# Kernel tuning notes

Measured on AMD Instinct MI355X. Metric: run time of the kernel, lower is better.

Reference implementation:

```python
import jax, jax.numpy as jnp
import numpy as np

VOCAB = 50000          # max binary columnId
N_NUM = 5000           # numerical feature ids = 1..5000
N_CAT = VOCAB + 1 - N_NUM  # categorical table rows (incl. padding row 0)
D = 128
B, L = 512, 512


def setup_inputs() -> dict:
    key = jax.random.key(0)
    k1, k2, k3, k4, k5 = jax.random.split(key, 5)
    feature_ids = jax.random.randint(k1, (B, L), 0, VOCAB + 1)
    feature_values = jax.random.normal(k2, (B, L), dtype=jnp.float32)
    cat_table = jax.random.normal(k3, (N_CAT, D), dtype=jnp.float32) * 0.02
    cat_table = cat_table.at[0].set(0.0)  # padding_idx=0
    num_weight = jax.random.normal(k4, (N_NUM, D), dtype=jnp.float32) * 0.02
    num_bias = jax.random.normal(k5, (N_NUM, D), dtype=jnp.float32) * 0.02
    # lookup buffers, exactly as built in __init__ with numerical ids = 1..N_NUM
    input_to_numeric = np.zeros(VOCAB + 1, dtype=np.int64)
    num_ids = np.arange(1, N_NUM + 1)
    input_to_numeric[num_ids] = np.arange(1, N_NUM + 1)
    input_to_categorical = np.zeros(VOCAB + 1, dtype=np.int64)
    cat_ids = np.where(input_to_numeric == 0)[0]
    input_to_categorical[cat_ids[1:]] = np.arange(1, cat_ids.size)
    return {
        "feature_ids": feature_ids,
        "feature_values": feature_values,
        "cat_table": cat_table,
        "num_weight": num_weight,
        "num_bias": num_bias,
        "input_to_numeric": jnp.asarray(input_to_numeric),
        "input_to_categorical": jnp.asarray(input_to_categorical),
    }


def reference(feature_ids, feature_values, cat_table, num_weight, num_bias,
              input_to_numeric, input_to_categorical):
    # numerical mask: isin(feature_ids, numerical_feature_ids) == nonzero mapped idx
    n_idx = input_to_numeric[feature_ids]                 # [B,L], 1..N_NUM or 0
    numerical_mask = n_idx > 0                            # [B,L]
    # numerical path: weight[id] * value + bias[id]  (1-based mapped -> 0-based row)
    n_row = jnp.maximum(n_idx - 1, 0)                     # [B,L]
    num_emb = num_weight[n_row] * feature_values[..., None] + num_bias[n_row]  # [B,L,D]
    # categorical path: route numerical positions to padding id 0
    cat_features = jnp.where(numerical_mask, 0, feature_ids)
    c_idx = input_to_categorical[cat_features]            # [B,L]
    cat_emb = cat_table[c_idx]                            # [B,L,D]
    # merge
    return jnp.where(numerical_mask[..., None], num_emb, cat_emb)
```

## Files before the change

kernel.cpp:

```cpp
#include <hip/hip_runtime.h>


constexpr int D  = 128;
constexpr int BL = 512 * 512;
constexpr int POS_PER_WAVE  = 16;
constexpr int WAVES_PER_BLK = 4;
constexpr int POS_PER_BLK   = POS_PER_WAVE * WAVES_PER_BLK;

__global__ __launch_bounds__(256) void emb_kernel(
    const int*    __restrict__ feature_ids,
    const float*  __restrict__ feature_values,
    const float*  __restrict__ cat_table,
    const float*  __restrict__ num_weight,
    const float*  __restrict__ num_bias,
    float*        __restrict__ out)
{
    const int tid  = threadIdx.x;
    const int lane = tid & 63;
    const int wave = tid >> 6;
    const int wbase = blockIdx.x * POS_PER_BLK + wave * POS_PER_WAVE;

    const int  myp = lane & 15;
    const int  id  = feature_ids[wbase + myp];
    const float mv = feature_values[wbase + myp];
    const int route = (id >= 1 && id <= 5000) ? -id
                    : ((id > 5000) ? id - 5000 : 0);

    const int sub  = (lane & 31) * 4;
    const int half = lane >> 5;

    float4 av[8];
    float  sc[8];
    int    brow[8];
#pragma unroll
    for (int k = 0; k < 8; ++k) {
        const int   p  = k * 2 + half;
        const int   rt = __shfl(route, p);
        const float vv = __shfl(mv, p);
        const bool isnum = rt < 0;
        const int  row   = isnum ? (-rt - 1) : rt;
        const float* a   = (isnum ? num_weight : cat_table) + row * D + sub;
        av[k]   = *(const float4*)a;
        sc[k]   = isnum ? vv : 1.0f;
        brow[k] = isnum ? row : -1;
    }

    float4 bv[8];
#pragma unroll
    for (int k = 0; k < 8; ++k) {
        bv[k] = make_float4(0.f, 0.f, 0.f, 0.f);
        if (brow[k] >= 0)
            bv[k] = *(const float4*)(num_bias + brow[k] * D + sub);
    }

    float* const obase = out + (long long)wbase * D;
#pragma unroll
    for (int k = 0; k < 8; ++k) {
        float4 r;
        r.x = fmaf(av[k].x, sc[k], bv[k].x);
        r.y = fmaf(av[k].y, sc[k], bv[k].y);
        r.z = fmaf(av[k].z, sc[k], bv[k].z);
        r.w = fmaf(av[k].w, sc[k], bv[k].w);
        *(float4*)(obase + (k * 64 + lane) * 4) = r;
    }
}

extern "C" void kernel_launch(void* const* d_in, const int* in_sizes, int n_in,
                              void* d_out, int out_size, void* d_ws, size_t ws_size,
                              hipStream_t stream) {
    const int*   feature_ids    = (const int*)  d_in[0];
    const float* feature_values = (const float*)d_in[1];
    const float* cat_table      = (const float*)d_in[2];
    const float* num_weight     = (const float*)d_in[3];
    const float* num_bias       = (const float*)d_in[4];
    float*       out            = (float*)      d_out;

    const int blocks = BL / POS_PER_BLK;
    emb_kernel<<<blocks, 256, 0, stream>>>(
        feature_ids, feature_values, cat_table, num_weight, num_bias, out);
}
```

Before: 178.8 us.

## Prefetch embedding tables into cache with grid barrier before persistent gather

Switches to a fixed grid of 1024 blocks, each handling 256 positions over four 64-position sub-iterations. Before gathering, every thread streams a slice of the categorical, numeric weight and bias tables so the tables are warm in L2/MALL. A software grid barrier built on a global atomic counter, with a spin limit, then holds blocks until all have finished prefetching. The aim is to turn random gather reads into cache hits, at the cost of a full table read, a spin barrier that relies on all 1024 blocks being co-resident, and fewer blocks in flight.

```diff
diff --git a/kernel.cpp b/kernel.cpp
--- a/kernel.cpp
+++ b/kernel.cpp
@@ -3,11 +3,18 @@
 
 constexpr int D  = 128;
 constexpr int BL = 512 * 512;
-constexpr int POS_PER_WAVE  = 16;
-constexpr int WAVES_PER_BLK = 4;
-constexpr int POS_PER_BLK   = POS_PER_WAVE * WAVES_PER_BLK;
+constexpr int BLOCKS   = 1024;
+constexpr int THREADS  = 256;
+constexpr int POS_PER_BLOCK = BL / BLOCKS;
+constexpr int POS_PER_WAVE  = POS_PER_BLOCK / 4;
+constexpr int GRID_THREADS  = BLOCKS * THREADS;
 
-__global__ __launch_bounds__(256) void emb_kernel(
+constexpr int CAT_F4 = 45001 * (D / 4);
+constexpr int NUM_F4 = 5000  * (D / 4);
+
+__device__ unsigned g_arrive = 0;
+
+__global__ __launch_bounds__(256, 4) void emb_kernel(
     const int*    __restrict__ feature_ids,
     const float*  __restrict__ feature_values,
     const float*  __restrict__ cat_table,
@@ -18,50 +25,82 @@
     const int tid  = threadIdx.x;
     const int lane = tid & 63;
     const int wave = tid >> 6;
-    const int wbase = blockIdx.x * POS_PER_BLK + wave * POS_PER_WAVE;
+    const int gtid = blockIdx.x * THREADS + tid;
 
-    const int  myp = lane & 15;
-    const int  id  = feature_ids[wbase + myp];
-    const float mv = feature_values[wbase + myp];
+    const int wpos0 = blockIdx.x * POS_PER_BLOCK + wave * POS_PER_WAVE;
+    const int   id = feature_ids[wpos0 + lane];
+    const float mv = feature_values[wpos0 + lane];
     const int route = (id >= 1 && id <= 5000) ? -id
                     : ((id > 5000) ? id - 5000 : 0);
+
+    {
+        float acc = 0.0f;
+        const float4* ct = (const float4*)cat_table;
+#pragma unroll
+        for (int i = 0; i < 6; ++i) {
+            const int j = gtid + i * GRID_THREADS;
+            if (j < CAT_F4) { float4 w = ct[j]; acc += w.x + w.w; }
+        }
+        if (gtid < NUM_F4) {
+            float4 w = ((const float4*)num_weight)[gtid];
+            float4 b = ((const float4*)num_bias)[gtid];
+            acc += w.x + w.w + b.x + b.w;
+        }
+        asm volatile("" :: "v"(acc));
+    }
+
+    __syncthreads();
+    if (tid == 0) {
+        const unsigned old    = atomicAdd(&g_arrive, 1u);
+        const unsigned target = ((old >> 10) + 1u) << 10;
+        int spins = 0;
+        while (__hip_atomic_load(&g_arrive, __ATOMIC_RELAXED,
+                                 __HIP_MEMORY_SCOPE_AGENT) < target
+               && spins < 65536) {
+            ++spins;
+            __builtin_amdgcn_s_sleep(2);
+        }
+    }
+    __syncthreads();
 
     const int sub  = (lane & 31) * 4;
     const int half = lane >> 5;
 
-    float4 av[8];
-    float  sc[8];
-    int    brow[8];
+    for (int m = 0; m < 4; ++m) {
+        float4 av[8];
+        float  sc[8];
+        int    brow[8];
 #pragma unroll
-    for (int k = 0; k < 8; ++k) {
-        const int   p  = k * 2 + half;
-        const int   rt = __shfl(route, p);
-        const float vv = __shfl(mv, p);
-        const bool isnum = rt < 0;
-        const int  row   = isnum ? (-rt - 1) : rt;
-        const float* a   = (isnum ? num_weight : cat_table) + row * D + sub;
-        av[k]   = *(const float4*)a;
-        sc[k]   = isnum ? vv : 1.0f;
-        brow[k] = isnum ? row : -1;
-    }
+        for (int k = 0; k < 8; ++k) {
+            const int   p  = m * 16 + k * 2 + half;
+            const int   rt = __shfl(route, p);
+            const float vv = __shfl(mv, p);
+            const bool isnum = rt < 0;
+            const int  row   = isnum ? (-rt - 1) : rt;
+            const float* a   = (isnum ? num_weight : cat_table) + row * D + sub;
+            av[k]   = *(const float4*)a;
+            sc[k]   = isnum ? vv : 1.0f;
+            brow[k] = isnum ? row : -1;
+        }
 
-    float4 bv[8];
+        float4 bv[8];
 #pragma unroll
-    for (int k = 0; k < 8; ++k) {
-        bv[k] = make_float4(0.f, 0.f, 0.f, 0.f);
-        if (brow[k] >= 0)
-            bv[k] = *(const float4*)(num_bias + brow[k] * D + sub);
-    }
+        for (int k = 0; k < 8; ++k) {
+            bv[k] = make_float4(0.f, 0.f, 0.f, 0.f);
+            if (brow[k] >= 0)
+                bv[k] = *(const float4*)(num_bias + brow[k] * D + sub);
+        }
 
-    float* const obase = out + (long long)wbase * D;
+        float* const obase = out + (long long)(wpos0 + m * 16) * D;
 #pragma unroll
-    for (int k = 0; k < 8; ++k) {
-        float4 r;
-        r.x = fmaf(av[k].x, sc[k], bv[k].x);
-        r.y = fmaf(av[k].y, sc[k], bv[k].y);
-        r.z = fmaf(av[k].z, sc[k], bv[k].z);
-        r.w = fmaf(av[k].w, sc[k], bv[k].w);
-        *(float4*)(obase + (k * 64 + lane) * 4) = r;
+        for (int k = 0; k < 8; ++k) {
+            float4 r;
+            r.x = fmaf(av[k].x, sc[k], bv[k].x);
+            r.y = fmaf(av[k].y, sc[k], bv[k].y);
+            r.z = fmaf(av[k].z, sc[k], bv[k].z);
+            r.w = fmaf(av[k].w, sc[k], bv[k].w);
+            *(float4*)(obase + (k * 64 + lane) * 4) = r;
+        }
     }
 }
 
@@ -75,7 +114,6 @@
     const float* num_bias       = (const float*)d_in[4];
     float*       out            = (float*)      d_out;
 
-    const int blocks = BL / POS_PER_BLK;
-    emb_kernel<<<blocks, 256, 0, stream>>>(
+    emb_kernel<<<BLOCKS, THREADS, 0, stream>>>(
         feature_ids, feature_values, cat_table, num_weight, num_bias, out);
 }
```

Result: slower. 211.2 us (+18.1%).
